# Performance work log

Hardware: AMD Instinct MI355X
Metric: run time of the kernel (lower is better)

The kernel has to match this reference:

```python
import jax, jax.numpy as jnp
import numpy as np

TOKENS = 32768
DIM = 2048
N_EXPERTS = 64
TOP_K = 6
ROUTE_SCALE = 1.0


def setup_inputs() -> dict:
    key = jax.random.key(0)
    k1, k2, k3 = jax.random.split(key, 3)
    x = jax.random.normal(k1, (TOKENS, DIM), dtype=jnp.float32)
    weight = jax.random.normal(k2, (N_EXPERTS, DIM), dtype=jnp.float32) * (1.0 / np.sqrt(DIM))
    bias = jax.random.normal(k3, (N_EXPERTS,), dtype=jnp.float32) * 0.01
    return {"x": x, "weight": weight, "bias": bias}


def reference(x, weight, bias):
    # scores = F.linear(x, weight): [T, E]
    logits = jnp.einsum('td,ed->te', x, weight)
    # softmax in float32 (score_func == 'softmax')
    original_scores = jax.nn.softmax(logits.astype(jnp.float32), axis=-1)
    # bias only affects expert selection, not the returned weights
    biased = original_scores + bias
    _, indices = jax.lax.top_k(biased, TOP_K)  # [T, top_k]
    weights = jnp.take_along_axis(original_scores, indices, axis=-1)
    weights = weights * ROUTE_SCALE
    return weights.astype(x.dtype), indices
```

## Files before the change

kernel.cpp:

```cpp
#include <hip/hip_runtime.h>
#include <hip/hip_bf16.h>
#include <math.h>

#define TOKENS 32768
#define DIM    2048
#define NEXP   64
#define TOPK   6

#define BM  128
#define BK  32
#define NIT (DIM / BK)
#define BMP 132
#define BEP 68

#define XS_SZ (BK * BMP)
#define WS_OFF (2 * XS_SZ)
#define WS_SZ (BK * BEP)
#define SMEM_FLOATS (2 * XS_SZ + 2 * WS_SZ)

__global__ __launch_bounds__(512, 2)
void gate_kernel(const float* __restrict__ x,
                 const float* __restrict__ w,
                 const float* __restrict__ bias,
                 float* __restrict__ out)
{
    __shared__ float smem[SMEM_FLOATS];

    const int tid  = threadIdx.x;
    const int tx   = tid & 15;
    const int ty   = tid >> 4;
    const int tok0 = blockIdx.x * BM;

    const int sr = tid >> 3;
    const int sc = tid & 7;

    float acc[4][4];
#pragma unroll
    for (int i = 0; i < 4; ++i)
#pragma unroll
        for (int j = 0; j < 4; ++j) acc[i][j] = 0.f;

    const float* xrow0 = x + (long)(tok0 + sr) * DIM + sc * 4;
    const float* xrow1 = x + (long)(tok0 + sr + 64) * DIM + sc * 4;
    const float* wrow  = w + (long)sr * DIM + sc * 4;

    {
        float4 xa = *(const float4*)(xrow0);
        float4 xb = *(const float4*)(xrow1);
        float4 wv = *(const float4*)(wrow);
        float* xs = smem;
        float* ws = smem + WS_OFF;
#pragma unroll
        for (int j = 0; j < 4; ++j) {
            xs[(sc * 4 + j) * BMP + sr]      = ((const float*)&xa)[j];
            xs[(sc * 4 + j) * BMP + sr + 64] = ((const float*)&xb)[j];
            ws[(sc * 4 + j) * BEP + sr]      = ((const float*)&wv)[j];
        }
    }
    __syncthreads();

    for (int it = 0; it < NIT; ++it) {
        const int buf = it & 1;
        const float* xs = smem + buf * XS_SZ;
        const float* ws = smem + WS_OFF + buf * WS_SZ;

        float4 xa, xb, wv;
        const bool more = (it + 1 < NIT);
        if (more) {
            const int k0 = (it + 1) * BK;
            xa = *(const float4*)(xrow0 + k0);
            xb = *(const float4*)(xrow1 + k0);
            wv = *(const float4*)(wrow  + k0);
        }

#pragma unroll
        for (int k = 0; k < BK; ++k) {
            const float4 a = *(const float4*)(xs + k * BMP + ty * 4);
            const float4 b = *(const float4*)(ws + k * BEP + tx * 4);
#pragma unroll
            for (int i = 0; i < 4; ++i) {
#pragma unroll
                for (int j = 0; j < 4; ++j)
                    acc[i][j] = fmaf(((const float*)&a)[i],
                                     ((const float*)&b)[j], acc[i][j]);
            }
        }

        if (more) {
            float* nxs = smem + (buf ^ 1) * XS_SZ;
            float* nws = smem + WS_OFF + (buf ^ 1) * WS_SZ;
#pragma unroll
            for (int j = 0; j < 4; ++j) {
                nxs[(sc * 4 + j) * BMP + sr]      = ((const float*)&xa)[j];
                nxs[(sc * 4 + j) * BMP + sr + 64] = ((const float*)&xb)[j];
                nws[(sc * 4 + j) * BEP + sr]      = ((const float*)&wv)[j];
            }
        }
        __syncthreads();
    }

    float* red = smem;
#pragma unroll
    for (int i = 0; i < 4; ++i)
#pragma unroll
        for (int j = 0; j < 4; ++j)
            red[(ty * 4 + i) * BEP + (tx * 4 + j)] = acc[i][j];
    __syncthreads();

    if (tid < BM) {
        const int m = tid;
        float lg[NEXP];
#pragma unroll
        for (int e = 0; e < NEXP; ++e) lg[e] = red[m * BEP + e];

        float mx = lg[0];
#pragma unroll
        for (int e = 1; e < NEXP; ++e) mx = fmaxf(mx, lg[e]);

        float sc4[NEXP];
        float sum = 0.f;
#pragma unroll
        for (int e = 0; e < NEXP; ++e) { sc4[e] = __expf(lg[e] - mx); sum += sc4[e]; }
        const float inv = 1.0f / sum;

        float bz[NEXP];
#pragma unroll
        for (int e = 0; e < NEXP; ++e) {
            sc4[e] *= inv;
            bz[e]  = sc4[e] + bias[e];
        }

        const int tok = tok0 + m;
        float* wout = out + (long)tok * TOPK;
        float* iout = out + (long)TOKENS * TOPK + (long)tok * TOPK;

        int win[TOPK];
#pragma unroll
        for (int p = 0; p < TOPK; ++p) {
            float bmax = -INFINITY;
            int   best = 0;
            float bsc  = 0.f;
#pragma unroll
            for (int e = 0; e < NEXP; ++e) {
                bool skip = false;
#pragma unroll
                for (int pp = 0; pp < p; ++pp) skip = skip || (e == win[pp]);
                float v = skip ? -INFINITY : bz[e];
                if (v > bmax) { bmax = v; best = e; bsc = sc4[e]; }
            }
            win[p]  = best;
            wout[p] = bsc;
            iout[p] = (float)best;
        }
    }
}

extern "C" void kernel_launch(void* const* d_in, const int* in_sizes, int n_in,
                              void* d_out, int out_size, void* d_ws, size_t ws_size,
                              hipStream_t stream) {
    const float* x = (const float*)d_in[0];
    const float* w = (const float*)d_in[1];
    const float* b = (const float*)d_in[2];
    float* out = (float*)d_out;

    dim3 grid(TOKENS / BM);
    dim3 block(512);
    gate_kernel<<<grid, block, 0, stream>>>(x, w, b, out);
}
```

Before: 403.3 us.

## Replace FP32 FMA GEMM with 3-way bf16-split MFMA emulation

Replaces the scalar FP32 FMA tiling with MFMA 16x16x32 bf16 instructions. Each fp32 operand is split into high, mid and low bf16 parts, and six cross products are accumulated to approximate fp32 precision. Tile shape changes to 64 tokens by 64 K with 256 threads, and x and w are converted in registers before being staged to LDS. The LDS double buffering is dropped in favour of a single buffer with register prefetch, and W is re-split in every block, which adds conversion ALU work and a small precision risk for top-k ties.

After: 386.2 us. -4.3%, faster.

```diff
diff --git a/kernel.cpp b/kernel.cpp
--- a/kernel.cpp
+++ b/kernel.cpp
@@ -7,111 +7,143 @@
 #define NEXP   64
 #define TOPK   6
 
-#define BM  128
-#define BK  32
-#define NIT (DIM / BK)
-#define BMP 132
-#define BEP 68
-
-#define XS_SZ (BK * BMP)
-#define WS_OFF (2 * XS_SZ)
-#define WS_SZ (BK * BEP)
-#define SMEM_FLOATS (2 * XS_SZ + 2 * WS_SZ)
-
-__global__ __launch_bounds__(512, 2)
+#define BM   64
+#define BK   64
+#define NIT  (DIM / BK)
+#define ST   72
+#define PLANE (BM * ST)
+
+typedef float f32x4 __attribute__((ext_vector_type(4)));
+typedef short sh8  __attribute__((ext_vector_type(8)));
+
+__device__ __forceinline__ ushort f2bf(float f) {
+    union { __hip_bfloat16 b; ushort u; } c;
+    c.b = __float2bfloat16(f);
+    return c.u;
+}
+__device__ __forceinline__ float bf2f(ushort u) {
+    union { ushort u; __hip_bfloat16 b; } c;
+    c.u = u;
+    return __bfloat162float(c.b);
+}
+
+__global__ __launch_bounds__(256, 2)
 void gate_kernel(const float* __restrict__ x,
                  const float* __restrict__ w,
                  const float* __restrict__ bias,
                  float* __restrict__ out)
 {
-    __shared__ float smem[SMEM_FLOATS];
+    __shared__ __align__(16) short smem[6 * PLANE];
 
     const int tid  = threadIdx.x;
-    const int tx   = tid & 15;
-    const int ty   = tid >> 4;
+    const int wave = tid >> 6;
+    const int lane = tid & 63;
+    const int quad = lane >> 4;
+    const int l15  = lane & 15;
     const int tok0 = blockIdx.x * BM;
 
-    const int sr = tid >> 3;
-    const int sc = tid & 7;
-
-    float acc[4][4];
-#pragma unroll
-    for (int i = 0; i < 4; ++i)
-#pragma unroll
-        for (int j = 0; j < 4; ++j) acc[i][j] = 0.f;
-
-    const float* xrow0 = x + (long)(tok0 + sr) * DIM + sc * 4;
-    const float* xrow1 = x + (long)(tok0 + sr + 64) * DIM + sc * 4;
-    const float* wrow  = w + (long)sr * DIM + sc * 4;
-
-    {
-        float4 xa = *(const float4*)(xrow0);
-        float4 xb = *(const float4*)(xrow1);
-        float4 wv = *(const float4*)(wrow);
-        float* xs = smem;
-        float* ws = smem + WS_OFF;
-#pragma unroll
-        for (int j = 0; j < 4; ++j) {
-            xs[(sc * 4 + j) * BMP + sr]      = ((const float*)&xa)[j];
-            xs[(sc * 4 + j) * BMP + sr + 64] = ((const float*)&xb)[j];
-            ws[(sc * 4 + j) * BEP + sr]      = ((const float*)&wv)[j];
-        }
+    const int sr = tid >> 2;
+    const int sq = tid & 3;
+
+    const float* xg = x + (long)(tok0 + sr) * DIM + sq * 16;
+    const float* wg = w + (long)sr * DIM + sq * 16;
+
+    f32x4 acc[4];
+#pragma unroll
+    for (int nt = 0; nt < 4; ++nt) acc[nt] = (f32x4){0.f, 0.f, 0.f, 0.f};
+
+    float4 xf[4], wf[4];
+
+    auto stage = [&]() {
+        const int base = sr * ST + sq * 16;
+#pragma unroll
+        for (int g = 0; g < 2; ++g) {
+            sh8 xh, xm, xl, wh, wm, wl;
+#pragma unroll
+            for (int i = 0; i < 8; ++i) {
+                {
+                    float f = ((const float*)&xf[g * 2])[i];
+                    ushort h = f2bf(f);  float r1 = f - bf2f(h);
+                    ushort m = f2bf(r1); float r2 = r1 - bf2f(m);
+                    ushort l = f2bf(r2);
+                    xh[i] = (short)h; xm[i] = (short)m; xl[i] = (short)l;
+                }
+                {
+                    float f = ((const float*)&wf[g * 2])[i];
+                    ushort h = f2bf(f);  float r1 = f - bf2f(h);
+                    ushort m = f2bf(r1); float r2 = r1 - bf2f(m);
+                    ushort l = f2bf(r2);
+                    wh[i] = (short)h; wm[i] = (short)m; wl[i] = (short)l;
+                }
+            }
+            *(sh8*)&smem[0 * PLANE + base + g * 8] = xh;
+            *(sh8*)&smem[1 * PLANE + base + g * 8] = xm;
+            *(sh8*)&smem[2 * PLANE + base + g * 8] = xl;
+            *(sh8*)&smem[3 * PLANE + base + g * 8] = wh;
+            *(sh8*)&smem[4 * PLANE + base + g * 8] = wm;
+            *(sh8*)&smem[5 * PLANE + base + g * 8] = wl;
+        }
+    };
+
+#pragma unroll
+    for (int j = 0; j < 4; ++j) {
+        xf[j] = *(const float4*)(xg + j * 4);
+        wf[j] = *(const float4*)(wg + j * 4);
     }
-    __syncthreads();
 
     for (int it = 0; it < NIT; ++it) {
-        const int buf = it & 1;
-        const float* xs = smem + buf * XS_SZ;
-        const float* ws = smem + WS_OFF + buf * WS_SZ;
-
-        float4 xa, xb, wv;
-        const bool more = (it + 1 < NIT);
-        if (more) {
+        stage();
+        __syncthreads();
+
+        if (it + 1 < NIT) {
             const int k0 = (it + 1) * BK;
-            xa = *(const float4*)(xrow0 + k0);
-            xb = *(const float4*)(xrow1 + k0);
-            wv = *(const float4*)(wrow  + k0);
-        }
-
-#pragma unroll
-        for (int k = 0; k < BK; ++k) {
-            const float4 a = *(const float4*)(xs + k * BMP + ty * 4);
-            const float4 b = *(const float4*)(ws + k * BEP + tx * 4);
-#pragma unroll
-            for (int i = 0; i < 4; ++i) {
-#pragma unroll
-                for (int j = 0; j < 4; ++j)
-                    acc[i][j] = fmaf(((const float*)&a)[i],
-                                     ((const float*)&b)[j], acc[i][j]);
-            }
-        }
-
-        if (more) {
-            float* nxs = smem + (buf ^ 1) * XS_SZ;
-            float* nws = smem + WS_OFF + (buf ^ 1) * WS_SZ;
 #pragma unroll
             for (int j = 0; j < 4; ++j) {
-                nxs[(sc * 4 + j) * BMP + sr]      = ((const float*)&xa)[j];
-                nxs[(sc * 4 + j) * BMP + sr + 64] = ((const float*)&xb)[j];
-                nws[(sc * 4 + j) * BEP + sr]      = ((const float*)&wv)[j];
+                xf[j] = *(const float4*)(xg + k0 + j * 4);
+                wf[j] = *(const float4*)(wg + k0 + j * 4);
+            }
+        }
+
+        const int arow = (wave * 16 + l15) * ST;
+#pragma unroll
+        for (int ks = 0; ks < 2; ++ks) {
+            const int kof = ks * 32 + quad * 8;
+            sh8 ah = *(const sh8*)&smem[0 * PLANE + arow + kof];
+            sh8 am = *(const sh8*)&smem[1 * PLANE + arow + kof];
+            sh8 al = *(const sh8*)&smem[2 * PLANE + arow + kof];
+#pragma unroll
+            for (int nt = 0; nt < 4; ++nt) {
+                const int brow = (nt * 16 + l15) * ST;
+                sh8 bh = *(const sh8*)&smem[3 * PLANE + brow + kof];
+                sh8 bm = *(const sh8*)&smem[4 * PLANE + brow + kof];
+                sh8 bl = *(const sh8*)&smem[5 * PLANE + brow + kof];
+                acc[nt] = __builtin_amdgcn_mfma_f32_16x16x32_bf16(ah, bh, acc[nt], 0, 0, 0);
+                acc[nt] = __builtin_amdgcn_mfma_f32_16x16x32_bf16(am, bh, acc[nt], 0, 0, 0);
+                acc[nt] = __builtin_amdgcn_mfma_f32_16x16x32_bf16(ah, bm, acc[nt], 0, 0, 0);
+                acc[nt] = __builtin_amdgcn_mfma_f32_16x16x32_bf16(al, bh, acc[nt], 0, 0, 0);
+                acc[nt] = __builtin_amdgcn_mfma_f32_16x16x32_bf16(am, bm, acc[nt], 0, 0, 0);
+                acc[nt] = __builtin_amdgcn_mfma_f32_16x16x32_bf16(ah, bl, acc[nt], 0, 0, 0);
             }
         }
         __syncthreads();
     }
 
-    float* red = smem;
-#pragma unroll
-    for (int i = 0; i < 4; ++i)
-#pragma unroll
-        for (int j = 0; j < 4; ++j)
-            red[(ty * 4 + i) * BEP + (tx * 4 + j)] = acc[i][j];
+    float* red = (float*)smem;
+#pragma unroll
+    for (int nt = 0; nt < 4; ++nt)
+#pragma unroll
+        for (int j = 0; j < 4; ++j) {
+            const int row = wave * 16 + quad * 4 + j;
+            const int col = nt * 16 + l15;
+            red[row * 69 + col] = acc[nt][j];
+        }
     __syncthreads();
 
     if (tid < BM) {
         const int m = tid;
         float lg[NEXP];
 #pragma unroll
-        for (int e = 0; e < NEXP; ++e) lg[e] = red[m * BEP + e];
+        for (int e = 0; e < NEXP; ++e) lg[e] = red[m * 69 + e];
 
         float mx = lg[0];
 #pragma unroll
@@ -164,6 +196,6 @@
     float* out = (float*)d_out;
 
     dim3 grid(TOKENS / BM);
-    dim3 block(512);
+    dim3 block(256);
     gate_kernel<<<grid, block, 0, stream>>>(x, w, b, out);
 }
```
